# Kernel tuning notes

Hardware: AMD Instinct MI355X
Metric: run time of the kernel (lower is better)

## Reference

```python
import jax, jax.numpy as jnp
import numpy as np

N_NODES = 100000
N_EDGES = 1000000
D = 64
N_GRAPHS = 128
N_LAYERS = 3
BN_EPS = 1e-5


def setup_inputs() -> dict:
    key = jax.random.key(0)
    ks = jax.random.split(key, 8)
    x = jax.random.normal(ks[0], (N_NODES, D), dtype=jnp.float32)
    edge_index = jax.random.randint(ks[1], (2, N_EDGES), 0, N_NODES, dtype=jnp.int64)
    edge_attr = jax.random.uniform(ks[2], (N_EDGES,), dtype=jnp.float32)
    batch = jnp.sort(jax.random.randint(ks[3], (N_NODES,), 0, N_GRAPHS, dtype=jnp.int64))
    # xavier-uniform linear weights [L, out, in], zero conv bias (PyG GCNConv adds bias after aggregation)
    limit = float(np.sqrt(6.0 / (D + D)))
    W = jax.random.uniform(ks[4], (N_LAYERS, D, D), minval=-limit, maxval=limit, dtype=jnp.float32)
    b = jnp.zeros((N_LAYERS, D), dtype=jnp.float32)
    prelu_a = jnp.asarray(0.25, dtype=jnp.float32)  # single PReLU shared across layers
    bn_w = jnp.ones((N_LAYERS, D), dtype=jnp.float32)
    bn_b = jnp.zeros((N_LAYERS, D), dtype=jnp.float32)
    return {"x": x, "edge_index": edge_index, "edge_attr": edge_attr, "batch": batch,
            "W": W, "b": b, "prelu_a": prelu_a, "bn_w": bn_w, "bn_b": bn_b}


def reference(x, edge_index, edge_attr, batch, W, b, prelu_a, bn_w, bn_b):
    src, dst = edge_index[0], edge_index[1]
    h = x
    pooled = []
    for i in range(N_LAYERS):
        # GCNConv (normalize=False, add_self_loops=False): lin -> weighted scatter-add -> bias
        h = h @ W[i].T                                      # [N, D]
        msg = h[src] * edge_attr[:, None]                   # [E, D] gather + scale
        h = jax.ops.segment_sum(msg, dst, num_segments=N_NODES) + b[i]
        # shared PReLU
        h = jnp.where(h >= 0, h, prelu_a * h)
        # BatchNorm1d (training mode: biased batch stats over nodes)
        mean = jnp.mean(h, axis=0)
        var = jnp.mean((h - mean) ** 2, axis=0)
        h = (h - mean) * jax.lax.rsqrt(var + BN_EPS) * bn_w[i] + bn_b[i]
        pooled.append(jax.ops.segment_sum(h, batch, num_segments=N_GRAPHS))
    global_rep = jnp.concatenate(pooled, axis=1)            # [G, L*D]
    x_stack = pooled[-1]                                    # [G, D]
    return (global_rep, x_stack)
```

## Files before the change

### kernel.cpp

```cpp
#include <hip/hip_runtime.h>

#define NNODES 100000
#define NEDGES 1000000
#define DIM 64
#define NGRAPHS 128
#define NLAYERS 3
#define BN_EPS 1e-5f

#define BINSZ 8
#define NBINS 12500
#define GBLK 256
#define ECHUNK 3907
#define SLICES 4

#define OFF_EDGES   0
#define OFF_BINBASE 2000000
#define OFF_AGG     2012544
#define OFF_YBF     8412544
#define OFF_XBF     11612544
#define OFF_COUNTS  OFF_YBF
#define OFF_OFFS    OFF_XBF
#define OFF_BTOT    OFF_AGG
#define OFF_GSUM4   (OFF_AGG + 16384)
#define OFF_PQ4     (OFF_AGG + 65536)
#define OFF_SCALE   14812544
#define OFF_SHIFT   14812736
#define OFF_END     14812928

__device__ __forceinline__ unsigned pack_bf16(float a, float b) {
    unsigned ua = __float_as_uint(a), ub = __float_as_uint(b);
    ua = (ua + 0x7FFFu + ((ua >> 16) & 1u)) >> 16;
    ub = (ub + 0x7FFFu + ((ub >> 16) & 1u)) & 0xFFFF0000u;
    return ua | ub;
}


__global__ __launch_bounds__(1024) void count_kernel(const int* __restrict__ ei,
                                                     int* __restrict__ counts) {
    __shared__ int hist[NBINS];
    const int tid = threadIdx.x, blk = blockIdx.x;
    for (int i = tid; i < NBINS; i += 1024) hist[i] = 0;
    __syncthreads();
    const int e0 = blk * ECHUNK, e1 = min(NEDGES, e0 + ECHUNK);
    for (int e = e0 + tid; e < e1; e += 1024)
        atomicAdd(&hist[ei[NEDGES + e] >> 3], 1);
    __syncthreads();
    for (int bin = tid; bin < NBINS; bin += 1024)
        counts[bin * GBLK + blk] = hist[bin];
}

__global__ __launch_bounds__(256) void s1_kernel(const int* __restrict__ counts,
                                                 int* __restrict__ offs,
                                                 int* __restrict__ btot) {
    const int bin = blockIdx.x * 4 + (threadIdx.x >> 6);
    const int lane = threadIdx.x & 63;
    if (bin >= NBINS) return;
    int carry = 0;
    for (int q = 0; q < GBLK; q += 64) {
        const int v = counts[bin * GBLK + q + lane];
        int s = v;
        for (int off = 1; off < 64; off <<= 1) {
            int t = __shfl_up(s, off);
            if (lane >= off) s += t;
        }
        offs[bin * GBLK + q + lane] = carry + s - v;
        carry += __shfl(s, 63);
    }
    if (lane == 0) btot[bin] = carry;
}

__global__ __launch_bounds__(1024) void s2_kernel(const int* __restrict__ btot,
                                                  int* __restrict__ binBase) {
    __shared__ int wsum[16];
    const int t = threadIdx.x, wid = t >> 6, lane = t & 63;
    int running = 0;
    for (int b = 0; b < NBINS; b += 1024) {
        const int i = b + t;
        const int v = (i < NBINS) ? btot[i] : 0;
        int s = v;
        for (int off = 1; off < 64; off <<= 1) {
            int x = __shfl_up(s, off);
            if (lane >= off) s += x;
        }
        __syncthreads();
        if (lane == 63) wsum[wid] = s;
        __syncthreads();
        int pw = 0, tot = 0;
#pragma unroll
        for (int k = 0; k < 16; ++k) {
            const int x = wsum[k];
            tot += x;
            if (k < wid) pw += x;
        }
        if (i < NBINS) binBase[i] = running + pw + s - v;
        running += tot;
    }
    if (t == 0) binBase[NBINS] = running;
}

__global__ __launch_bounds__(1024) void scatter_kernel(const int* __restrict__ ei,
                                                       const float* __restrict__ ea,
                                                       const int* __restrict__ binBase,
                                                       const int* __restrict__ offs,
                                                       int2* __restrict__ edges) {
    __shared__ int cur[NBINS];
    const int tid = threadIdx.x, blk = blockIdx.x;
    for (int i = tid; i < NBINS; i += 1024)
        cur[i] = binBase[i] + offs[i * GBLK + blk];
    __syncthreads();
    const int e0 = blk * ECHUNK, e1 = min(NEDGES, e0 + ECHUNK);
    for (int e = e0 + tid; e < e1; e += 1024) {
        const int dst = ei[NEDGES + e];
        const int src = ei[e];
        const float w = ea[e];
        const int pos = atomicAdd(&cur[dst >> 3], 1);
        edges[pos] = make_int2((src << 3) | (dst & (BINSZ - 1)), __float_as_int(w));
    }
}

__global__ __launch_bounds__(1024) void bounds_kernel(const int* __restrict__ batch,
                                                      int* __restrict__ endv) {
    const int i = blockIdx.x * 1024 + threadIdx.x;
    if (i >= NNODES) return;
    const int b0 = batch[i];
    const int b1 = (i + 1 < NNODES) ? batch[i + 1] : NGRAPHS;
    for (int g = b0; g < b1; ++g) endv[g] = i + 1;
    if (i == 0)
        for (int g = 0; g < b0; ++g) endv[g] = 0;
}

__global__ __launch_bounds__(256) void tobf_kernel(const float* __restrict__ x,
                                                   unsigned* __restrict__ xbf) {
    const int i = blockIdx.x * 256 + threadIdx.x;
    if (i >= NNODES * 32) return;
    const float2 v = *(const float2*)(x + (size_t)i * 2);
    xbf[i] = pack_bf16(v.x, v.y);
}

template <bool FIRST>
__global__ __launch_bounds__(256) void agg_kernel(const unsigned* __restrict__ hbf,
                                                  const float* __restrict__ scale,
                                                  const float* __restrict__ shift,
                                                  const int* __restrict__ binBase,
                                                  const int2* __restrict__ edges,
                                                  float* __restrict__ agg) {
    __shared__ float accAll[4][2][BINSZ * 64];
    const int w = threadIdx.x >> 6, lane = threadIdx.x & 63;
    const int bin = blockIdx.x * 4 + w;
    if (bin >= NBINS) return;
    const int half = lane >> 5, p = lane & 31, c0 = 2 * p;
    float* ac = accAll[w][half];
#pragma unroll
    for (int r = 0; r < BINSZ; ++r) *(float2*)&ac[r * 64 + c0] = make_float2(0.f, 0.f);
    float sc0 = 1.f, sc1 = 1.f, sh0 = 0.f, sh1 = 0.f;
    if (!FIRST) { sc0 = scale[c0]; sc1 = scale[c0 + 1]; sh0 = shift[c0]; sh1 = shift[c0 + 1]; }
    const int beg = binBase[bin], end = binBase[bin + 1];
    for (int j = beg; j < end; j += 64) {
        const int n = min(64, end - j);
        int2 ed = (j + lane < end) ? edges[j + lane] : make_int2(0, 0);
        const int n8 = n & ~7;
        int t = 0;
        for (; t < n8; t += 8) {
            int sd_[4]; float wt_[4]; unsigned u_[4];
#pragma unroll
            for (int q = 0; q < 4; ++q) {
                const int ii = t + 2 * q + half;
                sd_[q] = __shfl(ed.x, ii);
                wt_[q] = __int_as_float(__shfl(ed.y, ii));
            }
#pragma unroll
            for (int q = 0; q < 4; ++q) u_[q] = hbf[(size_t)(sd_[q] >> 3) * 32 + p];
#pragma unroll
            for (int q = 0; q < 4; ++q) {
                float h0 = __uint_as_float(u_[q] << 16);
                float h1 = __uint_as_float(u_[q] & 0xFFFF0000u);
                if (!FIRST) { h0 = fmaf(h0, sc0, sh0); h1 = fmaf(h1, sc1, sh1); }
                float2* a2 = (float2*)&ac[(sd_[q] & 7) * 64 + c0];
                float2 v = *a2;
                v.x = fmaf(wt_[q], h0, v.x);
                v.y = fmaf(wt_[q], h1, v.y);
                *a2 = v;
            }
        }
        for (; t < n; t += 2) {
            const int ii = min(t + half, n - 1);
            const int sd = __shfl(ed.x, ii);
            float wt = __int_as_float(__shfl(ed.y, ii));
            if (t + half >= n) wt = 0.f;
            const unsigned u = hbf[(size_t)(sd >> 3) * 32 + p];
            float h0 = __uint_as_float(u << 16);
            float h1 = __uint_as_float(u & 0xFFFF0000u);
            if (!FIRST) { h0 = fmaf(h0, sc0, sh0); h1 = fmaf(h1, sc1, sh1); }
            float2* a2 = (float2*)&ac[(sd & 7) * 64 + c0];
            float2 v = *a2;
            v.x = fmaf(wt, h0, v.x);
            v.y = fmaf(wt, h1, v.y);
            *a2 = v;
        }
    }
    const int nodeBase = bin * BINSZ;
#pragma unroll
    for (int r = 0; r < BINSZ; ++r)
        agg[(size_t)(nodeBase + r) * 64 + lane] =
            accAll[w][0][r * 64 + lane] + accAll[w][1][r * 64 + lane];
}

__global__ __launch_bounds__(256) void gemm_kernel(const float* __restrict__ agg,
                                                   const float* __restrict__ W,
                                                   const float* __restrict__ bias,
                                                   const float* __restrict__ pa_ptr,
                                                   unsigned* __restrict__ ybf) {
    __shared__ float As[128 * 68];
    __shared__ float Wt[64 * 68];
    const int tid = threadIdx.x;
    const int base = blockIdx.x * 128;
    for (int i = tid; i < 2048; i += 256) {
        const int r = i >> 4;
        const int q = (i & 15) * 4;
        const int row = base + r;
        float4 v = make_float4(0.f, 0.f, 0.f, 0.f);
        if (row < NNODES) v = *(const float4*)(agg + (size_t)row * 64 + q);
        *(float4*)&As[r * 68 + q] = v;
    }
    for (int i = tid; i < 4096; i += 256)
        Wt[(i & 63) * 68 + (i >> 6)] = W[i];
    __syncthreads();

    const int tc = tid & 7;
    const int tr = tid >> 3;
    float acc[4][8];
#pragma unroll
    for (int j = 0; j < 4; ++j)
#pragma unroll
        for (int c = 0; c < 8; ++c) acc[j][c] = 0.f;

    for (int kc = 0; kc < 16; ++kc) {
        const int k0 = kc * 4;
        float Af[4][4];
#pragma unroll
        for (int j = 0; j < 4; ++j) {
            const float4 t = *(const float4*)&As[(tr + 32 * j) * 68 + k0];
            Af[j][0] = t.x; Af[j][1] = t.y; Af[j][2] = t.z; Af[j][3] = t.w;
        }
#pragma unroll
        for (int kk = 0; kk < 4; ++kk) {
            const float4 w0 = *(const float4*)&Wt[(k0 + kk) * 68 + tc * 8];
            const float4 w1 = *(const float4*)&Wt[(k0 + kk) * 68 + tc * 8 + 4];
#pragma unroll
            for (int j = 0; j < 4; ++j) {
                const float a = Af[j][kk];
                acc[j][0] = fmaf(a, w0.x, acc[j][0]);
                acc[j][1] = fmaf(a, w0.y, acc[j][1]);
                acc[j][2] = fmaf(a, w0.z, acc[j][2]);
                acc[j][3] = fmaf(a, w0.w, acc[j][3]);
                acc[j][4] = fmaf(a, w1.x, acc[j][4]);
                acc[j][5] = fmaf(a, w1.y, acc[j][5]);
                acc[j][6] = fmaf(a, w1.z, acc[j][6]);
                acc[j][7] = fmaf(a, w1.w, acc[j][7]);
            }
        }
    }

    const float pa = *pa_ptr;
    const float4 b0 = *(const float4*)(bias + tc * 8);
    const float4 b1 = *(const float4*)(bias + tc * 8 + 4);
#pragma unroll
    for (int j = 0; j < 4; ++j) {
        const int row = base + tr + 32 * j;
        if (row >= NNODES) continue;
        float o[8];
        o[0] = acc[j][0] + b0.x; o[1] = acc[j][1] + b0.y;
        o[2] = acc[j][2] + b0.z; o[3] = acc[j][3] + b0.w;
        o[4] = acc[j][4] + b1.x; o[5] = acc[j][5] + b1.y;
        o[6] = acc[j][6] + b1.z; o[7] = acc[j][7] + b1.w;
#pragma unroll
        for (int c = 0; c < 8; ++c) o[c] = (o[c] >= 0.f) ? o[c] : pa * o[c];
        uint4 pk;
        pk.x = pack_bf16(o[0], o[1]);
        pk.y = pack_bf16(o[2], o[3]);
        pk.z = pack_bf16(o[4], o[5]);
        pk.w = pack_bf16(o[6], o[7]);
        *(uint4*)(ybf + (size_t)row * 32 + tc * 4) = pk;
    }
}

__global__ __launch_bounds__(256) void stats_kernel(const unsigned* __restrict__ ybf,
                                                    const int* __restrict__ endv,
                                                    float* __restrict__ gsum4,
                                                    float* __restrict__ pQ4) {
    __shared__ float red[2][8][64];
    const int g = blockIdx.x >> 2, s = blockIdx.x & 3;
    const int t = threadIdx.x, rl = t >> 5, p = t & 31, c0 = 2 * p;
    const int g0 = (g == 0) ? 0 : endv[g - 1];
    const int g1 = endv[g];
    const int len = g1 - g0;
    const int q0 = g0 + (len * s) / SLICES;
    const int q1 = g0 + (len * (s + 1)) / SLICES;
    float ga0 = 0.f, ga1 = 0.f, qq0 = 0.f, qq1 = 0.f;
    for (int r = q0 + rl; r < q1; r += 8) {
        const unsigned u = ybf[(size_t)r * 32 + p];
        const float f0 = __uint_as_float(u << 16);
        const float f1 = __uint_as_float(u & 0xFFFF0000u);
        ga0 += f0; ga1 += f1;
        qq0 = fmaf(f0, f0, qq0); qq1 = fmaf(f1, f1, qq1);
    }
    red[0][rl][c0] = ga0; red[0][rl][c0 + 1] = ga1;
    red[1][rl][c0] = qq0; red[1][rl][c0 + 1] = qq1;
    __syncthreads();
    if (rl == 0) {
        float a0 = 0.f, a1 = 0.f, b0 = 0.f, b1 = 0.f;
#pragma unroll
        for (int k = 0; k < 8; ++k) {
            a0 += red[0][k][c0]; a1 += red[0][k][c0 + 1];
            b0 += red[1][k][c0]; b1 += red[1][k][c0 + 1];
        }
        gsum4[blockIdx.x * 64 + c0] = a0; gsum4[blockIdx.x * 64 + c0 + 1] = a1;
        pQ4[blockIdx.x * 64 + c0] = b0;  pQ4[blockIdx.x * 64 + c0 + 1] = b1;
    }
}

__global__ __launch_bounds__(512) void finalize_kernel(const float* __restrict__ gsum4,
                                                       const float* __restrict__ pQ4,
                                                       const int* __restrict__ endv,
                                                       const float* __restrict__ bn_w,
                                                       const float* __restrict__ bn_b,
                                                       float* __restrict__ scale,
                                                       float* __restrict__ shift,
                                                       float* __restrict__ out, int layer) {
    __shared__ float rS[8][64], rQ[8][64];
    __shared__ float ssc[64], ssh[64];
    const int tid = threadIdx.x;
    const int c = tid & 63, pp = tid >> 6;
    float s = 0.f, q = 0.f;
    for (int sl = pp; sl < NGRAPHS * SLICES; sl += 8) {
        s += gsum4[sl * 64 + c];
        q += pQ4[sl * 64 + c];
    }
    rS[pp][c] = s; rQ[pp][c] = q;
    __syncthreads();
    if (tid < 64) {
        float S = 0.f, Q = 0.f;
#pragma unroll
        for (int k = 0; k < 8; ++k) { S += rS[k][c]; Q += rQ[k][c]; }
        const float mean = S * (1.f / NNODES);
        const float var = fmaxf(Q * (1.f / NNODES) - mean * mean, 0.f);
        const float inv = rsqrtf(var + BN_EPS);
        const float scv = inv * bn_w[c];
        const float shv = bn_b[c] - mean * scv;
        ssc[c] = scv; ssh[c] = shv;
        scale[c] = scv; shift[c] = shv;
    }
    __syncthreads();
    for (int idx = tid; idx < NGRAPHS * 64; idx += 512) {
        const int g = idx >> 6, ch = idx & 63;
        float gs = 0.f;
#pragma unroll
        for (int sl = 0; sl < SLICES; ++sl) gs += gsum4[(g * SLICES + sl) * 64 + ch];
        const int cnt = endv[g] - ((g == 0) ? 0 : endv[g - 1]);
        const float pooled = gs * ssc[ch] + (float)cnt * ssh[ch];
        out[g * (NLAYERS * 64) + layer * 64 + ch] = pooled;
        if (layer == NLAYERS - 1) out[NGRAPHS * NLAYERS * 64 + idx] = pooled;
    }
}

extern "C" void kernel_launch(void* const* d_in, const int* in_sizes, int n_in,
                              void* d_out, int out_size, void* d_ws, size_t ws_size,
                              hipStream_t stream) {
    const float* x     = (const float*)d_in[0];
    const int*   ei    = (const int*)d_in[1];
    const float* ea    = (const float*)d_in[2];
    const int*   batch = (const int*)d_in[3];
    const float* W     = (const float*)d_in[4];
    const float* b     = (const float*)d_in[5];
    const float* pa    = (const float*)d_in[6];
    const float* bn_w  = (const float*)d_in[7];
    const float* bn_b  = (const float*)d_in[8];
    float* out = (float*)d_out;
    float* ws  = (float*)d_ws;
    int*   wsi = (int*)d_ws;

    int2*     edges   = (int2*)(wsi + OFF_EDGES);
    int*      binBase = wsi + OFF_BINBASE;
    float*    agg     = ws + OFF_AGG;
    unsigned* ybf     = (unsigned*)(wsi + OFF_YBF);
    unsigned* xbf     = (unsigned*)(wsi + OFF_XBF);
    int*      counts  = wsi + OFF_COUNTS;
    int*      offs    = wsi + OFF_OFFS;
    int*      btot    = wsi + OFF_BTOT;
    float*    gsum4   = ws + OFF_GSUM4;
    float*    pQ4     = ws + OFF_PQ4;
    float*    scaleA  = ws + OFF_SCALE;
    float*    shiftA  = ws + OFF_SHIFT;
    int*      endv    = wsi + OFF_END;

    count_kernel<<<GBLK, 1024, 0, stream>>>(ei, counts);
    s1_kernel<<<(NBINS + 3) / 4, 256, 0, stream>>>(counts, offs, btot);
    s2_kernel<<<1, 1024, 0, stream>>>(btot, binBase);
    scatter_kernel<<<GBLK, 1024, 0, stream>>>(ei, ea, binBase, offs, edges);
    bounds_kernel<<<(NNODES + 1023) / 1024, 1024, 0, stream>>>(batch, endv);
    tobf_kernel<<<(NNODES * 32 + 255) / 256, 256, 0, stream>>>(x, xbf);

    for (int l = 0; l < NLAYERS; ++l) {
        if (l == 0)
            agg_kernel<true><<<(NBINS + 3) / 4, 256, 0, stream>>>(xbf, nullptr, nullptr,
                                                                  binBase, edges, agg);
        else
            agg_kernel<false><<<(NBINS + 3) / 4, 256, 0, stream>>>(ybf, scaleA + (l - 1) * 64,
                                                                   shiftA + (l - 1) * 64,
                                                                   binBase, edges, agg);
        gemm_kernel<<<(NNODES + 127) / 128, 256, 0, stream>>>(agg, W + l * 4096, b + l * 64,
                                                              pa, ybf);
        stats_kernel<<<NGRAPHS * SLICES, 256, 0, stream>>>(ybf, endv, gsum4, pQ4);
        finalize_kernel<<<1, 512, 0, stream>>>(gsum4, pQ4, endv, bn_w + l * 64,
                                               bn_b + l * 64, scaleA + l * 64,
                                               shiftA + l * 64, out, l);
    }
}
```

Measured before the change: 342.7 us.

## Fuse preprocessing kernels, use 16-bit bin counts, and unroll edge gather deeper

```diff
diff --git a/kernel.cpp b/kernel.cpp
--- a/kernel.cpp
+++ b/kernel.cpp
@@ -18,14 +18,14 @@
 #define OFF_AGG     2012544
 #define OFF_YBF     8412544
 #define OFF_XBF     11612544
-#define OFF_COUNTS  OFF_YBF
-#define OFF_OFFS    OFF_XBF
-#define OFF_BTOT    OFF_AGG
-#define OFF_GSUM4   (OFF_AGG + 16384)
-#define OFF_PQ4     (OFF_AGG + 65536)
-#define OFF_SCALE   14812544
-#define OFF_SHIFT   14812736
-#define OFF_END     14812928
+#define OFF_CNT     14812544
+#define OFF_OFS     16412544
+#define OFF_BTOT    18012544
+#define OFF_GSUM4   18025088
+#define OFF_PQ4     18057856
+#define OFF_SCALE   18090624
+#define OFF_SHIFT   18090816
+#define OFF_END     18091008
 
 __device__ __forceinline__ unsigned pack_bf16(float a, float b) {
     unsigned ua = __float_as_uint(a), ub = __float_as_uint(b);
@@ -34,9 +34,12 @@
     return ua | ub;
 }
 
-
 __global__ __launch_bounds__(1024) void count_kernel(const int* __restrict__ ei,
-                                                     int* __restrict__ counts) {
+                                                     const float* __restrict__ x,
+                                                     const int* __restrict__ batch,
+                                                     unsigned short* __restrict__ counts,
+                                                     unsigned* __restrict__ xbf,
+                                                     int* __restrict__ endv) {
     __shared__ int hist[NBINS];
     const int tid = threadIdx.x, blk = blockIdx.x;
     for (int i = tid; i < NBINS; i += 1024) hist[i] = 0;
@@ -45,28 +48,35 @@
     for (int e = e0 + tid; e < e1; e += 1024)
         atomicAdd(&hist[ei[NEDGES + e] >> 3], 1);
     __syncthreads();
+    unsigned short* crow = counts + (size_t)blk * NBINS;
     for (int bin = tid; bin < NBINS; bin += 1024)
-        counts[bin * GBLK + blk] = hist[bin];
-}
-
-__global__ __launch_bounds__(256) void s1_kernel(const int* __restrict__ counts,
-                                                 int* __restrict__ offs,
+        crow[bin] = (unsigned short)hist[bin];
+    const int gtid = blk * 1024 + tid;
+    for (int i = gtid; i < NNODES * 32; i += GBLK * 1024) {
+        const float2 v = *(const float2*)(x + (size_t)i * 2);
+        xbf[i] = pack_bf16(v.x, v.y);
+    }
+    for (int i = gtid; i < NNODES; i += GBLK * 1024) {
+        const int b0 = batch[i];
+        const int b1 = (i + 1 < NNODES) ? batch[i + 1] : NGRAPHS;
+        for (int g = b0; g < b1; ++g) endv[g] = i + 1;
+        if (i == 0)
+            for (int g = 0; g < b0; ++g) endv[g] = 0;
+    }
+}
+
+__global__ __launch_bounds__(256) void s1_kernel(const unsigned short* __restrict__ counts,
+                                                 unsigned short* __restrict__ offs,
                                                  int* __restrict__ btot) {
-    const int bin = blockIdx.x * 4 + (threadIdx.x >> 6);
-    const int lane = threadIdx.x & 63;
+    const int bin = blockIdx.x * 256 + threadIdx.x;
     if (bin >= NBINS) return;
-    int carry = 0;
-    for (int q = 0; q < GBLK; q += 64) {
-        const int v = counts[bin * GBLK + q + lane];
-        int s = v;
-        for (int off = 1; off < 64; off <<= 1) {
-            int t = __shfl_up(s, off);
-            if (lane >= off) s += t;
-        }
-        offs[bin * GBLK + q + lane] = carry + s - v;
-        carry += __shfl(s, 63);
-    }
-    if (lane == 0) btot[bin] = carry;
+    int run = 0;
+    for (int blk = 0; blk < GBLK; ++blk) {
+        const int v = counts[(size_t)blk * NBINS + bin];
+        offs[(size_t)blk * NBINS + bin] = (unsigned short)run;
+        run += v;
+    }
+    btot[bin] = run;
 }
 
 __global__ __launch_bounds__(1024) void s2_kernel(const int* __restrict__ btot,
@@ -101,12 +111,13 @@
 __global__ __launch_bounds__(1024) void scatter_kernel(const int* __restrict__ ei,
                                                        const float* __restrict__ ea,
                                                        const int* __restrict__ binBase,
-                                                       const int* __restrict__ offs,
+                                                       const unsigned short* __restrict__ offs,
                                                        int2* __restrict__ edges) {
     __shared__ int cur[NBINS];
     const int tid = threadIdx.x, blk = blockIdx.x;
+    const unsigned short* orow = offs + (size_t)blk * NBINS;
     for (int i = tid; i < NBINS; i += 1024)
-        cur[i] = binBase[i] + offs[i * GBLK + blk];
+        cur[i] = binBase[i] + (int)orow[i];
     __syncthreads();
     const int e0 = blk * ECHUNK, e1 = min(NEDGES, e0 + ECHUNK);
     for (int e = e0 + tid; e < e1; e += 1024) {
@@ -116,25 +127,6 @@
         const int pos = atomicAdd(&cur[dst >> 3], 1);
         edges[pos] = make_int2((src << 3) | (dst & (BINSZ - 1)), __float_as_int(w));
     }
-}
-
-__global__ __launch_bounds__(1024) void bounds_kernel(const int* __restrict__ batch,
-                                                      int* __restrict__ endv) {
-    const int i = blockIdx.x * 1024 + threadIdx.x;
-    if (i >= NNODES) return;
-    const int b0 = batch[i];
-    const int b1 = (i + 1 < NNODES) ? batch[i + 1] : NGRAPHS;
-    for (int g = b0; g < b1; ++g) endv[g] = i + 1;
-    if (i == 0)
-        for (int g = 0; g < b0; ++g) endv[g] = 0;
-}
-
-__global__ __launch_bounds__(256) void tobf_kernel(const float* __restrict__ x,
-                                                   unsigned* __restrict__ xbf) {
-    const int i = blockIdx.x * 256 + threadIdx.x;
-    if (i >= NNODES * 32) return;
-    const float2 v = *(const float2*)(x + (size_t)i * 2);
-    xbf[i] = pack_bf16(v.x, v.y);
 }
 
 template <bool FIRST>
@@ -147,7 +139,6 @@
     __shared__ float accAll[4][2][BINSZ * 64];
     const int w = threadIdx.x >> 6, lane = threadIdx.x & 63;
     const int bin = blockIdx.x * 4 + w;
-    if (bin >= NBINS) return;
     const int half = lane >> 5, p = lane & 31, c0 = 2 * p;
     float* ac = accAll[w][half];
 #pragma unroll
@@ -158,20 +149,20 @@
     for (int j = beg; j < end; j += 64) {
         const int n = min(64, end - j);
         int2 ed = (j + lane < end) ? edges[j + lane] : make_int2(0, 0);
-        const int n8 = n & ~7;
+        const int n16 = n & ~15;
         int t = 0;
-        for (; t < n8; t += 8) {
-            int sd_[4]; float wt_[4]; unsigned u_[4];
-#pragma unroll
-            for (int q = 0; q < 4; ++q) {
+        for (; t < n16; t += 16) {
+            int sd_[8]; float wt_[8]; unsigned u_[8];
+#pragma unroll
+            for (int q = 0; q < 8; ++q) {
                 const int ii = t + 2 * q + half;
                 sd_[q] = __shfl(ed.x, ii);
                 wt_[q] = __int_as_float(__shfl(ed.y, ii));
             }
 #pragma unroll
-            for (int q = 0; q < 4; ++q) u_[q] = hbf[(size_t)(sd_[q] >> 3) * 32 + p];
-#pragma unroll
-            for (int q = 0; q < 4; ++q) {
+            for (int q = 0; q < 8; ++q) u_[q] = hbf[(size_t)(sd_[q] >> 3) * 32 + p];
+#pragma unroll
+            for (int q = 0; q < 8; ++q) {
                 float h0 = __uint_as_float(u_[q] << 16);
                 float h1 = __uint_as_float(u_[q] & 0xFFFF0000u);
                 if (!FIRST) { h0 = fmaf(h0, sc0, sh0); h1 = fmaf(h1, sc1, sh1); }
@@ -379,35 +370,33 @@
     float* ws  = (float*)d_ws;
     int*   wsi = (int*)d_ws;
 
-    int2*     edges   = (int2*)(wsi + OFF_EDGES);
-    int*      binBase = wsi + OFF_BINBASE;
-    float*    agg     = ws + OFF_AGG;
-    unsigned* ybf     = (unsigned*)(wsi + OFF_YBF);
-    unsigned* xbf     = (unsigned*)(wsi + OFF_XBF);
-    int*      counts  = wsi + OFF_COUNTS;
-    int*      offs    = wsi + OFF_OFFS;
-    int*      btot    = wsi + OFF_BTOT;
-    float*    gsum4   = ws + OFF_GSUM4;
-    float*    pQ4     = ws + OFF_PQ4;
-    float*    scaleA  = ws + OFF_SCALE;
-    float*    shiftA  = ws + OFF_SHIFT;
-    int*      endv    = wsi + OFF_END;
-
-    count_kernel<<<GBLK, 1024, 0, stream>>>(ei, counts);
-    s1_kernel<<<(NBINS + 3) / 4, 256, 0, stream>>>(counts, offs, btot);
+    int2*           edges   = (int2*)(wsi + OFF_EDGES);
+    int*            binBase = wsi + OFF_BINBASE;
+    float*          agg     = ws + OFF_AGG;
+    unsigned*       ybf     = (unsigned*)(wsi + OFF_YBF);
+    unsigned*       xbf     = (unsigned*)(wsi + OFF_XBF);
+    unsigned short* counts  = (unsigned short*)(wsi + OFF_CNT);
+    unsigned short* offs    = (unsigned short*)(wsi + OFF_OFS);
+    int*            btot    = wsi + OFF_BTOT;
+    float*          gsum4   = ws + OFF_GSUM4;
+    float*          pQ4     = ws + OFF_PQ4;
+    float*          scaleA  = ws + OFF_SCALE;
+    float*          shiftA  = ws + OFF_SHIFT;
+    int*            endv    = wsi + OFF_END;
+
+    count_kernel<<<GBLK, 1024, 0, stream>>>(ei, x, batch, counts, xbf, endv);
+    s1_kernel<<<(NBINS + 255) / 256, 256, 0, stream>>>(counts, offs, btot);
     s2_kernel<<<1, 1024, 0, stream>>>(btot, binBase);
     scatter_kernel<<<GBLK, 1024, 0, stream>>>(ei, ea, binBase, offs, edges);
-    bounds_kernel<<<(NNODES + 1023) / 1024, 1024, 0, stream>>>(batch, endv);
-    tobf_kernel<<<(NNODES * 32 + 255) / 256, 256, 0, stream>>>(x, xbf);
 
     for (int l = 0; l < NLAYERS; ++l) {
         if (l == 0)
-            agg_kernel<true><<<(NBINS + 3) / 4, 256, 0, stream>>>(xbf, nullptr, nullptr,
-                                                                  binBase, edges, agg);
+            agg_kernel<true><<<NBINS / 4, 256, 0, stream>>>(xbf, nullptr, nullptr,
+                                                            binBase, edges, agg);
         else
-            agg_kernel<false><<<(NBINS + 3) / 4, 256, 0, stream>>>(ybf, scaleA + (l - 1) * 64,
-                                                                   shiftA + (l - 1) * 64,
-                                                                   binBase, edges, agg);
+            agg_kernel<false><<<NBINS / 4, 256, 0, stream>>>(ybf, scaleA + (l - 1) * 64,
+                                                             shiftA + (l - 1) * 64,
+                                                             binBase, edges, agg);
         gemm_kernel<<<(NNODES + 127) / 128, 256, 0, stream>>>(agg, W + l * 4096, b + l * 64,
                                                               pa, ybf);
         stats_kernel<<<NGRAPHS * SLICES, 256, 0, stream>>>(ybf, endv, gsum4, pQ4);
```

Result: faster. 309.6 us (-9.7%).
